# Kernel optimization log

Hardware: AMD Instinct MI355X
Metric: run time of the kernel (lower is better)

The kernel has to match this reference:

```python
import jax, jax.numpy as jnp
import numpy as np

ROPE_THETA = 10000.0

def _apply_rope(x, theta=ROPE_THETA):
    # x: [B, H, L, d_head]
    L, d_k = x.shape[-2], x.shape[-1]
    inv_freq = 1.0 / (theta ** (jnp.arange(0, d_k, 2, dtype=jnp.float32) / d_k))  # [d_k/2]
    ang = jnp.arange(L, dtype=jnp.float32)[:, None] * inv_freq[None, :]           # [L, d_k/2]
    ang = jnp.repeat(ang, 2, axis=-1)                                             # [L, d_k] interleaved
    xr = x.reshape(x.shape[:-1] + (d_k // 2, 2))
    rot = jnp.stack((-xr[..., 1], xr[..., 0]), axis=-1).reshape(x.shape)
    return x * jnp.cos(ang) + rot * jnp.sin(ang)

def setup_inputs() -> dict:
    key = jax.random.key(0)
    k1, k2, k3 = jax.random.split(key, 3)
    B, L, D = 2, 2048, 2048
    std_qkv = np.sqrt(2.0 / (D + 3 * D)).astype(np.float32)
    std_o = np.sqrt(2.0 / (D + D)).astype(np.float32)
    return {
        "x": jax.random.normal(k1, (B, L, D), dtype=jnp.float32),
        "W_qkv": jax.random.normal(k2, (3 * D, D), dtype=jnp.float32) * std_qkv,
        "W_o": jax.random.normal(k3, (D, D), dtype=jnp.float32) * std_o,
    }

def reference(x, W_qkv, W_o):
    B, L, D = x.shape
    H = 16
    dh = D // H
    qkv = jnp.einsum('bld,ed->ble', x, W_qkv)            # [B, L, 3D]
    q, k, v = jnp.split(qkv, 3, axis=-1)
    # [B, H, L, dh]
    q = q.reshape(B, L, H, dh).transpose(0, 2, 1, 3)
    k = k.reshape(B, L, H, dh).transpose(0, 2, 1, 3)
    v = v.reshape(B, L, H, dh).transpose(0, 2, 1, 3)
    q = _apply_rope(q)
    k = _apply_rope(k)
    scale = 1.0 / np.sqrt(dh).astype(np.float32)
    att = jnp.einsum('bhqd,bhkd->bhqk', q, k) * scale    # [B, H, L, L]
    causal = jnp.tril(jnp.ones((L, L), dtype=bool))
    att = jnp.where(causal, att, -jnp.inf)
    p = jax.nn.softmax(att, axis=-1)
    y = jnp.einsum('bhqk,bhkd->bhqd', p, v)              # [B, H, L, dh]
    y = y.transpose(0, 2, 1, 3).reshape(B, L, D)
    return jnp.einsum('bld,ed->ble', y, W_o)
```

## Files before the change

kernel.cpp:

```cpp
#include <hip/hip_runtime.h>
#include <math.h>

typedef __bf16 bf16x8 __attribute__((ext_vector_type(8)));
typedef float f32x4 __attribute__((ext_vector_type(4)));
typedef unsigned short us8 __attribute__((ext_vector_type(8)));

#define B_ 2
#define L_ 2048
#define D_ 2048
#define H_ 16
#define DH 128

__device__ __forceinline__ unsigned short f2b(float f) {
  union { float f; unsigned u; } v; v.f = f;
  unsigned u = v.u;
  return (unsigned short)((u + 0x7fffu + ((u >> 16) & 1u)) >> 16);
}
__device__ __forceinline__ float b2f(unsigned short h) {
  union { unsigned u; float f; } v; v.u = ((unsigned)h) << 16;
  return v.f;
}

#define GLD16(g, l) __builtin_amdgcn_global_load_lds(                          \
    (const __attribute__((address_space(1))) void*)(g),                        \
    (__attribute__((address_space(3))) void*)(l), 16, 0, 0)

__global__ void f32_to_bf16(const float* __restrict__ in,
                            unsigned short* __restrict__ out, int n4) {
  int i = blockIdx.x * blockDim.x + threadIdx.x;
  const int stride = gridDim.x * blockDim.x;
  for (; i < n4; i += stride) {
    const float4 v = ((const float4*)in)[i];
    ushort4 o;
    o.x = f2b(v.x); o.y = f2b(v.y); o.z = f2b(v.z); o.w = f2b(v.w);
    ((ushort4*)out)[i] = o;
  }
}

template <bool OUT_BF16>
__global__ __launch_bounds__(256)
void gemm_bt(const unsigned short* __restrict__ A,
             const unsigned short* __restrict__ Bm,
             void* __restrict__ Cv, int M, int N, int K) {
  __shared__ unsigned short lA[128 * 32];
  __shared__ unsigned short lB[128 * 32];
  const int tid = threadIdx.x;
  const int wave = tid >> 6, lane = tid & 63;
  const int lo = lane & 15, hi = lane >> 4;
  const int wm = (wave >> 1) * 64, wn = (wave & 1) * 64;
  const int bm = blockIdx.y, bn = blockIdx.x;
  f32x4 acc[4][4] = {};
  const long aBase = (long)bm * 128 * K;
  const long bBase = (long)bn * 128 * K;
  for (int k0 = 0; k0 < K; k0 += 32) {
    __syncthreads();
#pragma unroll
    for (int j = 0; j < 2; ++j) {
      const int c = j * 256 + tid;
      const int row = c >> 2, cq = c & 3;
      const int lbase = (j * 256 + wave * 64) * 8;
      GLD16(A + aBase + (long)row * K + k0 + cq * 8, &lA[lbase]);
      GLD16(Bm + bBase + (long)row * K + k0 + cq * 8, &lB[lbase]);
    }
    __syncthreads();
    bf16x8 af[4], bfr[4];
#pragma unroll
    for (int mi = 0; mi < 4; ++mi)
      af[mi] = *(const bf16x8*)&lA[(wm + mi * 16 + lo) * 32 + hi * 8];
#pragma unroll
    for (int ni = 0; ni < 4; ++ni)
      bfr[ni] = *(const bf16x8*)&lB[(wn + ni * 16 + lo) * 32 + hi * 8];
#pragma unroll
    for (int mi = 0; mi < 4; ++mi)
#pragma unroll
      for (int ni = 0; ni < 4; ++ni)
        acc[mi][ni] = __builtin_amdgcn_mfma_f32_16x16x32_bf16(
            af[mi], bfr[ni], acc[mi][ni], 0, 0, 0);
  }
  const int r0 = bm * 128 + wm, c0 = bn * 128 + wn;
#pragma unroll
  for (int mi = 0; mi < 4; ++mi) {
#pragma unroll
    for (int r = 0; r < 4; ++r) {
      const long row = r0 + mi * 16 + hi * 4 + r;
#pragma unroll
      for (int ni = 0; ni < 4; ++ni) {
        const int col = c0 + ni * 16 + lo;
        if (OUT_BF16)
          ((unsigned short*)Cv)[row * N + col] = f2b(acc[mi][ni][r]);
        else
          ((float*)Cv)[row * N + col] = acc[mi][ni][r];
      }
    }
  }
}

__global__ void rope_qk(const unsigned short* __restrict__ qkv,
                        unsigned short* __restrict__ Qo,
                        unsigned short* __restrict__ Ko) {
  const int idx = blockIdx.x * 256 + threadIdx.x;
  const int i = idx & 63;
  const int l = (idx >> 6) & (L_ - 1);
  const int h = (idx >> 17) & (H_ - 1);
  const int b = idx >> 21;
  const float invf = exp2f(-(float)i * 0.20762050593045077f);
  const float ang = (float)l * invf;
  float sn, cs;
  sincosf(ang, &sn, &cs);
  const long base = ((long)b * L_ + l) * (3 * D_) + h * DH + 2 * i;
  const unsigned qin = *(const unsigned*)&qkv[base];
  const unsigned kin = *(const unsigned*)&qkv[base + D_];
  const float q0 = b2f((unsigned short)qin), q1 = b2f((unsigned short)(qin >> 16));
  const float k0 = b2f((unsigned short)kin), k1 = b2f((unsigned short)(kin >> 16));
  const float sc = 0.12751743f;
  const float qo0 = (q0 * cs - q1 * sn) * sc, qo1 = (q1 * cs + q0 * sn) * sc;
  const float ko0 = (k0 * cs - k1 * sn), ko1 = (k1 * cs + k0 * sn);
  const long oo = ((long)(b * H_ + h) * L_ + l) * DH + 2 * i;
  *(unsigned*)&Qo[oo] = (unsigned)f2b(qo0) | ((unsigned)f2b(qo1) << 16);
  *(unsigned*)&Ko[oo] = (unsigned)f2b(ko0) | ((unsigned)f2b(ko1) << 16);
}

__global__ __launch_bounds__(256)
void v_fragpack(const unsigned short* __restrict__ qkv,
                unsigned short* __restrict__ Vf) {
  const int lblk = blockIdx.x;
  const int bh = blockIdx.y;
  const int b = bh >> 4, h = bh & 15;
  __shared__ unsigned short tile[64 * 137];
  const int tid = threadIdx.x;
  const int l0 = lblk * 64;
#pragma unroll
  for (int j = 0; j < 4; ++j) {
    const int c = j * 256 + tid;
    const int row = c >> 4, col8 = c & 15;
    const us8 v = *(const us8*)&qkv[((long)b * L_ + l0 + row) * (3 * D_) +
                                    2 * D_ + h * DH + col8 * 8];
    unsigned short* dst = &tile[row * 137 + col8 * 8];
#pragma unroll
    for (int e = 0; e < 8; ++e) dst[e] = v[e];
  }
  __syncthreads();
#pragma unroll
  for (int j = 0; j < 4; ++j) {
    const int c = j * 256 + tid;
    const int k32l = c >> 9, t2 = (c >> 6) & 7, lane = c & 63;
    const int lo = lane & 15, hi = lane >> 4;
    us8 v;
#pragma unroll
    for (int e = 0; e < 8; ++e)
      v[e] = tile[(k32l * 32 + hi * 8 + e) * 137 + t2 * 16 + lo];
    *(us8*)&Vf[(((size_t)bh * 64 + lblk * 2 + k32l) * 8 + t2) * 512 + lane * 8] = v;
  }
}

__global__ __launch_bounds__(256, 2)
void flash_attn3(const unsigned short* __restrict__ Q,
                 const unsigned short* __restrict__ Kg,
                 const unsigned short* __restrict__ Vf,
                 unsigned short* __restrict__ Y) {
  const int p = blockIdx.x;
  const int tA = p, tB = (L_ / 64 - 1) - p;
  const int h = blockIdx.y, b = blockIdx.z;
  const int tid = threadIdx.x;
  const int wave = tid >> 6, lane = tid & 63;
  const int lo = lane & 15, hi = lane >> 4;
  const int swz = (lo & 7) << 4;
  const int qA = tA * 64 + wave * 16;
  const int qB = tB * 64 + wave * 16;
  const long hoff = ((long)(b * H_ + h)) * L_ * DH;
  const unsigned short* Qh = Q + hoff;
  const unsigned short* Kh = Kg + hoff;
  const unsigned short* Vfh = Vf + ((size_t)(b * H_ + h)) * (64 * 8 * 512);

  __shared__ unsigned short lK[2][64 * 128];
  __shared__ unsigned short pl[4][2][16 * 72];
  unsigned short* plA = &pl[wave][0][0];
  unsigned short* plB = &pl[wave][1][0];

  auto stage = [&](int bufi, int kv0s) {
    unsigned short* bk = &lK[bufi][0];
#pragma unroll
    for (int j = 0; j < 4; ++j) {
      const int c = j * 256 + tid;
      const int row = c >> 4;
      const int soff = ((c & 15) ^ (row & 7)) << 3;
      GLD16(Kh + (long)(kv0s + row) * DH + soff, &bk[(c & ~63) * 8]);
    }
  };

  bf16x8 qfA[4], qfB[4];
#pragma unroll
  for (int s = 0; s < 4; ++s) {
    qfA[s] = *(const bf16x8*)&Qh[(long)(qA + lo) * DH + s * 32 + hi * 8];
    qfB[s] = *(const bf16x8*)&Qh[(long)(qB + lo) * DH + s * 32 + hi * 8];
  }

  float mA = -INFINITY, lsA = 0.f, mB = -INFINITY, lsB = 0.f;
  f32x4 yA[8] = {}, yB[8] = {};

  auto softmax = [&](f32x4 (&st)[4], float& m, float& lsum, f32x4 (&yacc)[8],
                     unsigned short* plw, int qw, int kv0) {
    if (kv0 + 63 > qw) {
      const int d0 = qw + lo - kv0 - hi * 4;
#pragma unroll
      for (int t = 0; t < 4; ++t) {
        const int dt = d0 - t * 16;
#pragma unroll
        for (int r = 0; r < 4; ++r)
          if (r > dt) st[t][r] = -INFINITY;
      }
    }
    float tm0 = fmaxf(fmaxf(st[0][0], st[0][1]), fmaxf(st[0][2], st[0][3]));
    float tm1 = fmaxf(fmaxf(st[1][0], st[1][1]), fmaxf(st[1][2], st[1][3]));
    float tm2 = fmaxf(fmaxf(st[2][0], st[2][1]), fmaxf(st[2][2], st[2][3]));
    float tm3 = fmaxf(fmaxf(st[3][0], st[3][1]), fmaxf(st[3][2], st[3][3]));
    float rm = fmaxf(fmaxf(tm0, tm1), fmaxf(tm2, tm3));
    rm = fmaxf(rm, __shfl_xor(rm, 16));
    rm = fmaxf(rm, __shfl_xor(rm, 32));
    if (!__all(rm <= m + 8.f)) {
      const float mn = fmaxf(m, rm);
      const float alpha = exp2f(m - mn);
      m = mn;
      lsum *= alpha;
      float ar[4];
#pragma unroll
      for (int r = 0; r < 4; ++r) ar[r] = __shfl(alpha, hi * 4 + r);
#pragma unroll
      for (int t2 = 0; t2 < 8; ++t2)
#pragma unroll
        for (int r = 0; r < 4; ++r) yacc[t2][r] *= ar[r];
    }
    float rs = 0.f;
#pragma unroll
    for (int t = 0; t < 4; ++t) {
#pragma unroll
      for (int r2 = 0; r2 < 2; ++r2) {
        const float e0 = exp2f(st[t][2 * r2] - m);
        const float e1 = exp2f(st[t][2 * r2 + 1] - m);
        rs += e0 + e1;
        const unsigned short u0 = __builtin_bit_cast(unsigned short, (__bf16)e0);
        const unsigned short u1 = __builtin_bit_cast(unsigned short, (__bf16)e1);
        *(unsigned*)&plw[lo * 72 + t * 16 + hi * 4 + 2 * r2] =
            (unsigned)u0 | ((unsigned)u1 << 16);
      }
    }
    rs += __shfl_xor(rs, 16);
    rs += __shfl_xor(rs, 32);
    lsum += rs;
  };

  const int nIter = tB + 1;
  stage(0, 0);
  __syncthreads();

  for (int it = 0; it < nIter; ++it) {
    const int kv0 = it * 64;
    const bool aAct = (it <= tA);
    if (it + 1 < nIter) stage((it + 1) & 1, kv0 + 64);
    const char* bkc = (const char*)&lK[it & 1][0];
    f32x4 stA[4] = {}, stB[4] = {};
    if (aAct) {
#pragma unroll
      for (int s = 0; s < 4; ++s) {
        const int inner = (lo * 256 + s * 64 + hi * 16) ^ swz;
#pragma unroll
        for (int t = 0; t < 4; ++t) {
          const bf16x8 kf = *(const bf16x8*)(bkc + t * 4096 + inner);
          stA[t] = __builtin_amdgcn_mfma_f32_16x16x32_bf16(kf, qfA[s], stA[t], 0, 0, 0);
          stB[t] = __builtin_amdgcn_mfma_f32_16x16x32_bf16(kf, qfB[s], stB[t], 0, 0, 0);
        }
      }
    } else {
#pragma unroll
      for (int s = 0; s < 4; ++s) {
        const int inner = (lo * 256 + s * 64 + hi * 16) ^ swz;
#pragma unroll
        for (int t = 0; t < 4; ++t) {
          const bf16x8 kf = *(const bf16x8*)(bkc + t * 4096 + inner);
          stB[t] = __builtin_amdgcn_mfma_f32_16x16x32_bf16(kf, qfB[s], stB[t], 0, 0, 0);
        }
      }
    }
    if (aAct) softmax(stA, mA, lsA, yA, plA, qA, kv0);
    softmax(stB, mB, lsB, yB, plB, qB, kv0);
    const unsigned short* vbase = Vfh + (size_t)(it * 16) * 512 + lane * 8;
#pragma unroll
    for (int kt = 0; kt < 2; ++kt) {
      bf16x8 vf[8];
#pragma unroll
      for (int t2 = 0; t2 < 8; ++t2)
        vf[t2] = *(const bf16x8*)(vbase + (size_t)(kt * 8 + t2) * 512);
      const bf16x8 pfB = *(const bf16x8*)&plB[lo * 72 + kt * 32 + hi * 8];
#pragma unroll
      for (int t2 = 0; t2 < 8; ++t2)
        yB[t2] = __builtin_amdgcn_mfma_f32_16x16x32_bf16(pfB, vf[t2], yB[t2], 0, 0, 0);
      if (aAct) {
        const bf16x8 pfA = *(const bf16x8*)&plA[lo * 72 + kt * 32 + hi * 8];
#pragma unroll
        for (int t2 = 0; t2 < 8; ++t2)
          yA[t2] = __builtin_amdgcn_mfma_f32_16x16x32_bf16(pfA, vf[t2], yA[t2], 0, 0, 0);
      }
    }
    __syncthreads();
  }

  auto wout = [&](f32x4 (&yacc)[8], float lsum, int qw) {
    const float inv = 1.f / lsum;
    float ir[4];
#pragma unroll
    for (int r = 0; r < 4; ++r) ir[r] = __shfl(inv, hi * 4 + r);
#pragma unroll
    for (int r = 0; r < 4; ++r) {
      const long row = qw + hi * 4 + r;
      unsigned short* yrow = Y + ((long)b * L_ + row) * D_ + h * DH;
#pragma unroll
      for (int t2 = 0; t2 < 8; ++t2)
        yrow[t2 * 16 + lo] = f2b(yacc[t2][r] * ir[r]);
    }
  };
  wout(yA, lsA, qA);
  wout(yB, lsB, qB);
}

extern "C" void kernel_launch(void* const* d_in, const int* in_sizes, int n_in,
                              void* d_out, int out_size, void* d_ws, size_t ws_size,
                              hipStream_t stream) {
  const float* x = (const float*)d_in[0];
  const float* wqkv = (const float*)d_in[1];
  const float* wo = (const float*)d_in[2];
  float* out = (float*)d_out;

  unsigned short* ws = (unsigned short*)d_ws;
  const size_t N_X = (size_t)B_ * L_ * D_;
  const size_t N_WQKV = (size_t)3 * D_ * D_;
  const size_t N_WO = (size_t)D_ * D_;
  const size_t N_QKV = (size_t)B_ * L_ * 3 * D_;
  const size_t N_HEAD = (size_t)B_ * H_ * L_ * DH;
  unsigned short* xb = ws;
  unsigned short* wqkb = xb + N_X;
  unsigned short* wob = wqkb + N_WQKV;
  unsigned short* qkv = wob + N_WO;
  unsigned short* Qb = qkv + N_QKV;
  unsigned short* Kb = Qb + N_HEAD;
  unsigned short* Vf = Kb + N_HEAD;
  unsigned short* Yb = Vf + N_HEAD;
  const size_t need = (size_t)(Yb + N_HEAD - ws) * sizeof(unsigned short);
  if (ws_size < need) return;

  f32_to_bf16<<<2048, 256, 0, stream>>>(x, xb, (int)(N_X / 4));
  f32_to_bf16<<<2048, 256, 0, stream>>>(wqkv, wqkb, (int)(N_WQKV / 4));
  f32_to_bf16<<<2048, 256, 0, stream>>>(wo, wob, (int)(N_WO / 4));

  gemm_bt<true><<<dim3(3 * D_ / 128, B_ * L_ / 128), 256, 0, stream>>>(
      xb, wqkb, qkv, B_ * L_, 3 * D_, D_);

  rope_qk<<<(B_ * H_ * L_ * 64) / 256, 256, 0, stream>>>(qkv, Qb, Kb);
  v_fragpack<<<dim3(L_ / 64, B_ * H_), 256, 0, stream>>>(qkv, Vf);

  flash_attn3<<<dim3(16, H_, B_), 256, 0, stream>>>(Qb, Kb, Vf, Yb);

  gemm_bt<false><<<dim3(D_ / 128, B_ * L_ / 128), 256, 0, stream>>>(
      Yb, wob, out, B_ * L_, D_, D_);
}
```

Measured before the change: 323.7 us.

## Replace GEMM with 256x256 tile, 8-wave double-buffered pipelined kernel

Swaps the simple 128x128 single-buffered GEMM for a 512-thread kernel computing 256x256 tiles with BK=64. Global-to-LDS loads are double-buffered and interleaved with MFMA phases, using XOR-swizzled LDS layout, s_setprio around the MFMA bursts, and a remapped block order for L2 locality. The aim is to hide memory latency, cut LDS bank conflicts and raise data reuse in both projection GEMMs. In exchange it uses much more LDS and registers, which lowers occupancy, and its correctness depends on hand-placed vmcnt waits and barriers.

Result: faster. 296.4 us (-8.4%).

```diff
diff --git a/kernel.cpp b/kernel.cpp
--- a/kernel.cpp
+++ b/kernel.cpp
@@ -37,49 +37,125 @@
   }
 }
 
+
+#define SB()                              \
+  do {                                    \
+    __builtin_amdgcn_s_barrier();         \
+    __builtin_amdgcn_sched_barrier(0);    \
+  } while (0)
+
+#define VMC2() asm volatile("s_waitcnt vmcnt(2)" ::: "memory")
+
+#define LOAD_A(BUF, MH)                                                        \
+  _Pragma("unroll") for (int q = 0; q < 4; ++q) {                              \
+    const int rowA = (MH) * 64 + q * 16 + lo;                                  \
+    _Pragma("unroll") for (int kk = 0; kk < 2; ++kk)                           \
+        af[q][kk] = *(const bf16x8*)&lds[0][BUF][wmh]                          \
+            [rowA * 64 + ((kk * 4 + hi) ^ sw) * 8];                            \
+  }
+
+#define LOAD_B(BUF, NH)                                                        \
+  _Pragma("unroll") for (int j = 0; j < 2; ++j) {                              \
+    const int rowB = bro + ((NH) * 2 + j) * 16;                                \
+    _Pragma("unroll") for (int kk = 0; kk < 2; ++kk)                           \
+        bfr[j][kk] = *(const bf16x8*)&lds[1][BUF][bhalf]                       \
+            [rowB * 64 + ((kk * 4 + hi) ^ sw) * 8];                            \
+  }
+
+#define MFMA16(MH, NH)                                                         \
+  do {                                                                         \
+    __builtin_amdgcn_s_setprio(1);                                             \
+    _Pragma("unroll") for (int q = 0; q < 4; ++q) {                            \
+      _Pragma("unroll") for (int j = 0; j < 2; ++j) {                          \
+        acc[(MH) * 4 + q][(NH) * 2 + j] =                                      \
+            __builtin_amdgcn_mfma_f32_16x16x32_bf16(                           \
+                af[q][0], bfr[j][0], acc[(MH) * 4 + q][(NH) * 2 + j], 0, 0, 0);\
+        acc[(MH) * 4 + q][(NH) * 2 + j] =                                      \
+            __builtin_amdgcn_mfma_f32_16x16x32_bf16(                           \
+                af[q][1], bfr[j][1], acc[(MH) * 4 + q][(NH) * 2 + j], 0, 0, 0);\
+      }                                                                        \
+    }                                                                          \
+    __builtin_amdgcn_s_setprio(0);                                             \
+  } while (0)
+
 template <bool OUT_BF16>
-__global__ __launch_bounds__(256)
-void gemm_bt(const unsigned short* __restrict__ A,
-             const unsigned short* __restrict__ Bm,
-             void* __restrict__ Cv, int M, int N, int K) {
-  __shared__ unsigned short lA[128 * 32];
-  __shared__ unsigned short lB[128 * 32];
+__global__ __launch_bounds__(512)
+void gemm8p(const unsigned short* __restrict__ A,
+            const unsigned short* __restrict__ Bm,
+            void* __restrict__ Cv, int M, int N, int K) {
+  __shared__ __align__(16) unsigned short lds[2][2][2][128 * 64];
   const int tid = threadIdx.x;
-  const int wave = tid >> 6, lane = tid & 63;
-  const int lo = lane & 15, hi = lane >> 4;
-  const int wm = (wave >> 1) * 64, wn = (wave & 1) * 64;
-  const int bm = blockIdx.y, bn = blockIdx.x;
-  f32x4 acc[4][4] = {};
-  const long aBase = (long)bm * 128 * K;
-  const long bBase = (long)bn * 128 * K;
-  for (int k0 = 0; k0 < K; k0 += 32) {
-    __syncthreads();
-#pragma unroll
-    for (int j = 0; j < 2; ++j) {
-      const int c = j * 256 + tid;
-      const int row = c >> 2, cq = c & 3;
-      const int lbase = (j * 256 + wave * 64) * 8;
-      GLD16(A + aBase + (long)row * K + k0 + cq * 8, &lA[lbase]);
-      GLD16(Bm + bBase + (long)row * K + k0 + cq * 8, &lB[lbase]);
-    }
-    __syncthreads();
-    bf16x8 af[4], bfr[4];
-#pragma unroll
-    for (int mi = 0; mi < 4; ++mi)
-      af[mi] = *(const bf16x8*)&lA[(wm + mi * 16 + lo) * 32 + hi * 8];
-#pragma unroll
-    for (int ni = 0; ni < 4; ++ni)
-      bfr[ni] = *(const bf16x8*)&lB[(wn + ni * 16 + lo) * 32 + hi * 8];
-#pragma unroll
-    for (int mi = 0; mi < 4; ++mi)
-#pragma unroll
-      for (int ni = 0; ni < 4; ++ni)
-        acc[mi][ni] = __builtin_amdgcn_mfma_f32_16x16x32_bf16(
-            af[mi], bfr[ni], acc[mi][ni], 0, 0, 0);
-  }
-  const int r0 = bm * 128 + wm, c0 = bn * 128 + wn;
-#pragma unroll
-  for (int mi = 0; mi < 4; ++mi) {
+  const int w = tid >> 6, lane = tid & 63;
+  const int lo = lane & 15, hi = lane >> 4, sw = lo & 7;
+  const int wmh = w >> 2;
+  const int wn = (w & 3) * 64;
+  const int bhalf = wn >> 7, bro = (wn & 64) + lo;
+  const int GM = M >> 8;
+  const int nwg = gridDim.x;
+  const int f = blockIdx.x;
+  const int v = (f & 7) * (nwg >> 3) + (f >> 3);
+  const int bn = v / GM, bm = v % GM;
+  const int NI = K >> 7;
+
+  auto stageU = [&](int mat, int buf, int half, int tile) {
+    const unsigned short* G = mat ? Bm : A;
+    const int r256 = (mat ? bn : bm) * 256 + half * 128;
+#pragma unroll
+    for (int u = 0; u < 2; ++u) {
+      const int c = u * 512 + tid;
+      const int row = c >> 3;
+      const int gs = (c & 7) ^ (row & 7);
+      GLD16(G + (long)(r256 + row) * K + tile * 64 + gs * 8,
+            &lds[mat][buf][half][(u * 512 + (tid & ~63)) * 8]);
+    }
+  };
+
+  f32x4 acc[8][4] = {};
+  bf16x8 af[4][2], bfr[2][2];
+
+  stageU(0, 0, 0, 0); stageU(0, 0, 1, 0);
+  stageU(1, 0, 0, 0); stageU(1, 0, 1, 0);
+  stageU(0, 1, 0, 1);
+  VMC2();
+  SB();
+
+  for (int i = 0; i < NI; ++i) {
+    const int t1 = 2 * i + 1;
+    const bool nx = (i + 1 < NI);
+    LOAD_A(0, 0) LOAD_B(0, 0)
+    stageU(1, 1, 0, t1);
+    SB(); MFMA16(0, 0); SB();
+    LOAD_B(0, 1)
+    stageU(0, 1, 1, t1);
+    SB(); MFMA16(0, 1); SB();
+    LOAD_A(0, 1)
+    stageU(1, 1, 1, t1);
+    SB(); MFMA16(1, 1); SB();
+    LOAD_B(0, 0)
+    if (nx) stageU(0, 0, 0, t1 + 1);
+    SB(); MFMA16(1, 0);
+    VMC2();
+    SB();
+    LOAD_A(1, 0) LOAD_B(1, 0)
+    if (nx) stageU(0, 0, 1, t1 + 1);
+    SB(); MFMA16(0, 0); SB();
+    LOAD_B(1, 1)
+    if (nx) stageU(1, 0, 0, t1 + 1);
+    SB(); MFMA16(0, 1); SB();
+    LOAD_A(1, 1)
+    if (nx) stageU(1, 0, 1, t1 + 1);
+    SB(); MFMA16(1, 1); SB();
+    LOAD_B(1, 0)
+    if (nx) stageU(0, 1, 0, t1 + 2);
+    SB(); MFMA16(1, 0);
+    VMC2();
+    SB();
+  }
+
+  const int r0 = bm * 256 + wmh * 128;
+  const int c0 = bn * 256 + wn;
+#pragma unroll
+  for (int mi = 0; mi < 8; ++mi) {
 #pragma unroll
     for (int r = 0; r < 4; ++r) {
       const long row = r0 + mi * 16 + hi * 4 + r;
@@ -351,7 +427,7 @@
   f32_to_bf16<<<2048, 256, 0, stream>>>(wqkv, wqkb, (int)(N_WQKV / 4));
   f32_to_bf16<<<2048, 256, 0, stream>>>(wo, wob, (int)(N_WO / 4));
 
-  gemm_bt<true><<<dim3(3 * D_ / 128, B_ * L_ / 128), 256, 0, stream>>>(
+  gemm8p<true><<<(B_ * L_ / 256) * (3 * D_ / 256), 512, 0, stream>>>(
       xb, wqkb, qkv, B_ * L_, 3 * D_, D_);
 
   rope_qk<<<(B_ * H_ * L_ * 64) / 256, 256, 0, stream>>>(qkv, Qb, Kb);
@@ -359,6 +435,6 @@
 
   flash_attn3<<<dim3(16, H_, B_), 256, 0, stream>>>(Qb, Kb, Vf, Yb);
 
-  gemm_bt<false><<<dim3(D_ / 128, B_ * L_ / 128), 256, 0, stream>>>(
+  gemm8p<false><<<(B_ * L_ / 256) * (D_ / 256), 512, 0, stream>>>(
       Yb, wob, out, B_ * L_, D_, D_);
 }
```

## Replace GEMM with triple-buffered 128x256 swizzled-LDS pipelined kernel

Applied to the files above, without the earlier changes.

Replaces the simple single-buffered 128x128 GEMM with a 512-thread, 128x256-tile kernel. It uses triple-buffered LDS with a K-step of 64, XOR-swizzled LDS addressing to avoid bank conflicts, async global-to-LDS prefetch two tiles ahead using explicit vmcnt waits, and s_setprio around MFMA bursts. A grid remap groups workgroups for better L2 reuse. The goal is to hide load latency and cut the per-iteration barrier stalls of the old kernel, at the cost of much larger LDS use and lower occupancy.

Measured after the change: 290.6 us. 1.11x faster.

```diff
diff --git a/kernel.cpp b/kernel.cpp
--- a/kernel.cpp
+++ b/kernel.cpp
@@ -24,6 +24,11 @@
 #define GLD16(g, l) __builtin_amdgcn_global_load_lds(                          \
     (const __attribute__((address_space(1))) void*)(g),                        \
     (__attribute__((address_space(3))) void*)(l), 16, 0, 0)
+
+#define SBAR() __builtin_amdgcn_s_barrier()
+#define LGK0() asm volatile("s_waitcnt lgkmcnt(0)")
+#define VMC6() asm volatile("s_waitcnt vmcnt(6)" ::: "memory")
+#define VMC0() asm volatile("s_waitcnt vmcnt(0)" ::: "memory")
 
 __global__ void f32_to_bf16(const float* __restrict__ in,
                             unsigned short* __restrict__ out, int n4) {
@@ -38,46 +43,97 @@
 }
 
 template <bool OUT_BF16>
-__global__ __launch_bounds__(256)
-void gemm_bt(const unsigned short* __restrict__ A,
-             const unsigned short* __restrict__ Bm,
-             void* __restrict__ Cv, int M, int N, int K) {
-  __shared__ unsigned short lA[128 * 32];
-  __shared__ unsigned short lB[128 * 32];
+__global__ __launch_bounds__(512)
+void gemm3b(const unsigned short* __restrict__ A,
+            const unsigned short* __restrict__ Bm,
+            void* __restrict__ Cv, int M, int N, int K) {
+  __shared__ __align__(16) unsigned short lA[3][128 * 64];
+  __shared__ __align__(16) unsigned short lB[3][2][128 * 64];
   const int tid = threadIdx.x;
-  const int wave = tid >> 6, lane = tid & 63;
+  const int w = tid >> 6, lane = tid & 63;
   const int lo = lane & 15, hi = lane >> 4;
-  const int wm = (wave >> 1) * 64, wn = (wave & 1) * 64;
-  const int bm = blockIdx.y, bn = blockIdx.x;
+  const int mh = w >> 2;
+  const int wn = (w & 3) * 64;
+  const int bhalf = wn >> 7;
+  const int brb = (wn & 64) + lo;
+  const int GM = M >> 7;
+  const int nwg = gridDim.x;
+  const int f = blockIdx.x;
+  const int v = (f & 7) * (nwg >> 3) + (f >> 3);
+  const int bn = v / GM, bm = v % GM;
+  const int NT = K >> 6;
+
+  const int row64 = tid >> 3;
+  const int gs = (tid & 7) ^ (row64 & 7);
+  auto stA = [&](int buf, int u, int tile) {
+    GLD16(A + (long)(bm * 128 + u * 64 + row64) * K + tile * 64 + gs * 8,
+          &lA[buf][u * 4096 + (tid & ~63) * 8]);
+  };
+  auto stB = [&](int buf, int hf, int u, int tile) {
+    GLD16(Bm + (long)(bn * 256 + hf * 128 + u * 64 + row64) * K + tile * 64 + gs * 8,
+          &lB[buf][hf][u * 4096 + (tid & ~63) * 8]);
+  };
+
   f32x4 acc[4][4] = {};
-  const long aBase = (long)bm * 128 * K;
-  const long bBase = (long)bn * 128 * K;
-  for (int k0 = 0; k0 < K; k0 += 32) {
-    __syncthreads();
-#pragma unroll
-    for (int j = 0; j < 2; ++j) {
-      const int c = j * 256 + tid;
-      const int row = c >> 2, cq = c & 3;
-      const int lbase = (j * 256 + wave * 64) * 8;
-      GLD16(A + aBase + (long)row * K + k0 + cq * 8, &lA[lbase]);
-      GLD16(Bm + bBase + (long)row * K + k0 + cq * 8, &lB[lbase]);
-    }
-    __syncthreads();
-    bf16x8 af[4], bfr[4];
-#pragma unroll
-    for (int mi = 0; mi < 4; ++mi)
-      af[mi] = *(const bf16x8*)&lA[(wm + mi * 16 + lo) * 32 + hi * 8];
-#pragma unroll
-    for (int ni = 0; ni < 4; ++ni)
-      bfr[ni] = *(const bf16x8*)&lB[(wn + ni * 16 + lo) * 32 + hi * 8];
+
+  stA(0, 0, 0); stA(0, 1, 0);
+  stB(0, 0, 0, 0); stB(0, 0, 1, 0); stB(0, 1, 0, 0); stB(0, 1, 1, 0);
+  stA(1, 0, 1); stA(1, 1, 1);
+  stB(1, 0, 0, 1); stB(1, 0, 1, 1); stB(1, 1, 0, 1); stB(1, 1, 1, 1);
+  VMC6();
+  SBAR();
+
+  for (int t = 0; t < NT; ++t) {
+    const int bt = t % 3;
+    const int b2 = (t + 2) % 3;
+    const bool nx = (t + 2 < NT);
+    bf16x8 af[4], bf[4];
+#pragma unroll
+    for (int mi = 0; mi < 4; ++mi) {
+      const int r = mh * 64 + mi * 16 + lo;
+      af[mi] = *(const bf16x8*)&lA[bt][r * 64 + ((hi ^ (r & 7)) * 8)];
+    }
+#pragma unroll
+    for (int ni = 0; ni < 4; ++ni) {
+      const int rb = brb + ni * 16;
+      bf[ni] = *(const bf16x8*)&lB[bt][bhalf][rb * 64 + ((hi ^ (rb & 7)) * 8)];
+    }
+    if (nx) { stA(b2, 0, t + 2); stA(b2, 1, t + 2); stB(b2, 0, 0, t + 2); }
+    SBAR(); LGK0();
+    __builtin_amdgcn_s_setprio(1);
 #pragma unroll
     for (int mi = 0; mi < 4; ++mi)
 #pragma unroll
       for (int ni = 0; ni < 4; ++ni)
         acc[mi][ni] = __builtin_amdgcn_mfma_f32_16x16x32_bf16(
-            af[mi], bfr[ni], acc[mi][ni], 0, 0, 0);
-  }
-  const int r0 = bm * 128 + wm, c0 = bn * 128 + wn;
+            af[mi], bf[ni], acc[mi][ni], 0, 0, 0);
+    __builtin_amdgcn_s_setprio(0);
+#pragma unroll
+    for (int mi = 0; mi < 4; ++mi) {
+      const int r = mh * 64 + mi * 16 + lo;
+      af[mi] = *(const bf16x8*)&lA[bt][r * 64 + (((4 + hi) ^ (r & 7)) * 8)];
+    }
+#pragma unroll
+    for (int ni = 0; ni < 4; ++ni) {
+      const int rb = brb + ni * 16;
+      bf[ni] = *(const bf16x8*)&lB[bt][bhalf][rb * 64 + (((4 + hi) ^ (rb & 7)) * 8)];
+    }
+    if (nx) { stB(b2, 0, 1, t + 2); stB(b2, 1, 0, t + 2); stB(b2, 1, 1, t + 2); }
+    SBAR(); LGK0();
+    __builtin_amdgcn_s_setprio(1);
+#pragma unroll
+    for (int mi = 0; mi < 4; ++mi)
+#pragma unroll
+      for (int ni = 0; ni < 4; ++ni)
+        acc[mi][ni] = __builtin_amdgcn_mfma_f32_16x16x32_bf16(
+            af[mi], bf[ni], acc[mi][ni], 0, 0, 0);
+    __builtin_amdgcn_s_setprio(0);
+    if (t < NT - 2) VMC6(); else VMC0();
+    SBAR();
+  }
+
+  const int r0 = bm * 128 + mh * 64;
+  const int c0 = bn * 256 + wn;
 #pragma unroll
   for (int mi = 0; mi < 4; ++mi) {
 #pragma unroll
@@ -351,7 +407,7 @@
   f32_to_bf16<<<2048, 256, 0, stream>>>(wqkv, wqkb, (int)(N_WQKV / 4));
   f32_to_bf16<<<2048, 256, 0, stream>>>(wo, wob, (int)(N_WO / 4));
 
-  gemm_bt<true><<<dim3(3 * D_ / 128, B_ * L_ / 128), 256, 0, stream>>>(
+  gemm3b<true><<<(B_ * L_ / 128) * (3 * D_ / 256), 512, 0, stream>>>(
       xb, wqkb, qkv, B_ * L_, 3 * D_, D_);
 
   rope_qk<<<(B_ * H_ * L_ * 64) / 256, 256, 0, stream>>>(qkv, Qb, Kb);
@@ -359,6 +415,6 @@
 
   flash_attn3<<<dim3(16, H_, B_), 256, 0, stream>>>(Qb, Kb, Vf, Yb);
 
-  gemm_bt<false><<<dim3(D_ / 128, B_ * L_ / 128), 256, 0, stream>>>(
+  gemm3b<false><<<(B_ * L_ / 128) * (D_ / 256), 512, 0, stream>>>(
       Yb, wob, out, B_ * L_, D_, D_);
 }
```
